# Optimization experiments

Measured on AMD Instinct MI355X. Metric: run time of the kernel, lower is better.

The kernel has to match this reference:

```python
import jax, jax.numpy as jnp
import numpy as np

jax.config.update("jax_enable_x64", True)  # torch lfilter runs in double precision

SR = 24000
RES_SIZE = 64
R_MIN, R_MAX = 0.9999, 0.99999
B, T = 4, 120000


def setup_inputs() -> dict:
    # Probe coefficients (fixed buffers, computed exactly as in Probe.__init__)
    theta_min = 2 * np.pi * 10.0 / SR
    theta_max = 2 * np.pi * 100.0 / SR
    theta = np.exp(np.linspace(np.log(theta_min), np.log(theta_max), RES_SIZE))
    radii = np.linspace(R_MIN, R_MAX, RES_SIZE)
    a1 = -2.0 * radii * np.cos(theta)          # [C]
    a2 = radii ** 2                             # [C]
    b0 = (1.0 - radii) * 0.5                    # [C]

    # Tank mixing weight: orthogonal init, shape [out=64, in=128] (rows orthonormal)
    rng = np.random.default_rng(1337)
    q, _ = np.linalg.qr(rng.standard_normal((2 * RES_SIZE, RES_SIZE)))  # [128,64], orthonormal cols
    W = q.T.astype(np.float32)                  # [64,128]

    key = jax.random.key(0)
    k1, k2 = jax.random.split(key)
    pred = jax.random.normal(k1, (B, 1, T), dtype=jnp.float32)
    target = jax.random.normal(k2, (B, 1, T), dtype=jnp.float32)
    return {
        "pred": pred,
        "target": target,
        "a1": jnp.asarray(a1, jnp.float64),
        "a2": jnp.asarray(a2, jnp.float64),
        "b0": jnp.asarray(b0, jnp.float64),
        "W": jnp.asarray(W, jnp.float32),
    }


def _biquad_bank(x, a1, a2, b0):
    """Biquad filter bank. x: [N, T] float64; coeffs: [C]. Returns [N, C, T].
    y[t] = b0*x[t] - a1*y[t-1] - a2*y[t-2]  (a0 = 1, b1 = b2 = 0, clamp=False)
    """
    n = x.shape[0]
    c = a1.shape[0]

    def step(carry, xt):
        y1, y2 = carry  # each [N, C]
        y = b0[None, :] * xt[:, None] - a1[None, :] * y1 - a2[None, :] * y2
        return (y, y1), y

    init = (jnp.zeros((n, c), x.dtype), jnp.zeros((n, c), x.dtype))
    _, ys = jax.lax.scan(step, init, x.T)      # [T, N, C]
    return jnp.transpose(ys, (1, 2, 0))        # [N, C, T]


def _probe(x, a1, a2, b0):
    """x: [B,1,T] float -> [B, 2C, T] float32 (fwd state ++ bwd state)."""
    xs = x[:, 0, :].astype(jnp.float64)        # [B, T]
    # run forward-time and reversed-time filters in one batched scan
    both = jnp.concatenate([xs, xs[:, ::-1]], axis=0)       # [2B, T]
    ys = _biquad_bank(both, a1, a2, b0)                      # [2B, C, T]
    nb = xs.shape[0]
    fwd_state = ys[:nb]                                      # [B, C, T]
    bwd_state = ys[nb:][:, :, ::-1]                          # [B, C, T] (flipped back)
    return jnp.concatenate([fwd_state, bwd_state], axis=1).astype(jnp.float32)


def _tank(x, W):
    """x: [B, 2C, T], W: [C, 2C] -> tanh(W @ x): [B, C, T]."""
    return jnp.tanh(jnp.einsum("bct,oc->bot", x, W))


def reference(pred, target, a1, a2, b0, W):
    t = pred.shape[-1]
    margin = t // 3
    p_emb = _tank(_probe(pred, a1, a2, b0), W)    # [B, C, T]
    t_emb = _tank(_probe(target, a1, a2, b0), W)  # [B, C, T]
    p_valid = p_emb[..., margin:t - margin]
    t_valid = t_emb[..., margin:t - margin]
    return jnp.mean(jnp.abs(p_valid - t_valid))
```

## Files before the change

kernel.cpp:

```cpp
#include <hip/hip_runtime.h>

#define T_LEN 120000
#define LBLK 160
#define PBLK 750
#define PB_USED 500
#define SEG_LEN 25
#define NSEG_USED 20
#define CCH 32
#define NCHUNK 5
#define BATCH 4
#define K0 250
#define NKV 250
#define DENOM 20480000.0
#define YSTR 130

typedef _Float16 half8 __attribute__((ext_vector_type(8)));
typedef float f32x4 __attribute__((ext_vector_type(4)));

__device__ __forceinline__ float fast_tanh(float x) {
  float e = __expf(2.0f * x);
  return 1.0f - 2.0f / (e + 1.0f);
}

__device__ __forceinline__ bool coeffs_are_f64(const void* a2p) {
  double probe = *(const double*)a2p;
  return probe > 0.9 && probe < 1.0;
}
__device__ __forceinline__ double coeff_d(const void* p, bool f64, int ch) {
  return f64 ? ((const double*)p)[ch] : (double)((const float*)p)[ch];
}

__device__ __forceinline__ void mat_pow(double A1, double A2, int e,
                                        double& r00, double& r01,
                                        double& r10, double& r11) {
  double m00 = -A1, m01 = -A2, m10 = 1.0, m11 = 0.0;
  r00 = 1.0; r01 = 0.0; r10 = 0.0; r11 = 1.0;
  while (e) {
    if (e & 1) {
      double t00 = r00 * m00 + r01 * m10, t01 = r00 * m01 + r01 * m11;
      double t10 = r10 * m00 + r11 * m10, t11 = r10 * m01 + r11 * m11;
      r00 = t00; r01 = t01; r10 = t10; r11 = t11;
    }
    e >>= 1;
    if (e) {
      double t00 = m00 * m00 + m01 * m10, t01 = m00 * m01 + m01 * m11;
      double t10 = m10 * m00 + m11 * m10, t11 = m10 * m01 + m11 * m11;
      m00 = t00; m01 = t01; m10 = t10; m11 = t11;
    }
  }
}

__global__ __launch_bounds__(64) void pass1(
    const float* __restrict__ pred, const float* __restrict__ tgt,
    const void* a1p, const void* a2p, const void* b0p,
    double* __restrict__ fbuf, double* __restrict__ wsum)
{
  if ((blockIdx.x | blockIdx.y) == 0 && threadIdx.x == 0) {
    wsum[0] = 0.0;
    ((unsigned int*)(wsum + 1))[0] = 0u;
  }
  int k = blockIdx.x, r = blockIdx.y;
  int i = r >> 3, d = (r >> 2) & 1, b = r & 3;
  const float* sig = (i ? tgt : pred) + b * T_LEN;
  __shared__ float xs[LBLK];
  int base = k * LBLK;
  for (int j = threadIdx.x; j < LBLK; j += 64)
    xs[j] = d ? sig[T_LEN - 1 - (base + j)] : sig[base + j];
  __syncthreads();
  int ch = threadIdx.x;
  bool f64 = coeffs_are_f64(a2p);
  float A1 = (float)coeff_d(a1p, f64, ch);
  float A2 = (float)coeff_d(a2p, f64, ch);
  float B0 = (float)coeff_d(b0p, f64, ch);
  float y1 = 0.0f, y2 = 0.0f;
  for (int j = 0; j < LBLK; ++j) {
    float y = fmaf(-A1, y1, fmaf(-A2, y2, B0 * xs[j]));
    y2 = y1; y1 = y;
  }
  int s = r * 64 + ch;
  ((double2*)fbuf)[(size_t)k * 1024 + s] = make_double2((double)y1, (double)y2);
}

__global__ __launch_bounds__(64) void pass2a(
    const void* a1p, const void* a2p,
    const double* __restrict__ fbuf, double* __restrict__ sbuf)
{
  int seg = blockIdx.x >> 4;
  int s = ((blockIdx.x & 15) << 6) + threadIdx.x;
  int ch = s & 63;
  bool f64 = coeffs_are_f64(a2p);
  double r00, r01, r10, r11;
  mat_pow(coeff_d(a1p, f64, ch), coeff_d(a2p, f64, ch), LBLK, r00, r01, r10, r11);
  const double2* fb = (const double2*)fbuf;
  double y1 = 0.0, y2 = 0.0;
  for (int jj = 0; jj < SEG_LEN / 5; ++jj) {
    size_t kb = (size_t)(seg * SEG_LEN + jj * 5) * 1024 + s;
    double2 f0 = fb[kb], f1 = fb[kb + 1024], f2 = fb[kb + 2048],
            f3 = fb[kb + 3072], f4 = fb[kb + 4096];
    double n1, n2;
    n1 = r00*y1 + r01*y2 + f0.x; n2 = r10*y1 + r11*y2 + f0.y; y1=n1; y2=n2;
    n1 = r00*y1 + r01*y2 + f1.x; n2 = r10*y1 + r11*y2 + f1.y; y1=n1; y2=n2;
    n1 = r00*y1 + r01*y2 + f2.x; n2 = r10*y1 + r11*y2 + f2.y; y1=n1; y2=n2;
    n1 = r00*y1 + r01*y2 + f3.x; n2 = r10*y1 + r11*y2 + f3.y; y1=n1; y2=n2;
    n1 = r00*y1 + r01*y2 + f4.x; n2 = r10*y1 + r11*y2 + f4.y; y1=n1; y2=n2;
  }
  ((double2*)sbuf)[(size_t)seg * 1024 + s] = make_double2(y1, y2);
}

__global__ __launch_bounds__(256, 4) void pass3(
    const float* __restrict__ pred, const float* __restrict__ tgt,
    const void* a1p, const void* a2p, const void* b0p,
    const float* __restrict__ W, const double* __restrict__ fbuf,
    const double* __restrict__ sbuf, double* __restrict__ wsum,
    float* __restrict__ out)
{
  int k = K0 + blockIdx.x;
  int b = blockIdx.y;
  int tid = threadIdx.x;
  __shared__ __align__(16) _Float16 ys[2][64 * YSTR];
  __shared__ float red[4];

  int g = tid >> 6, lane = tid & 63;
  int gu = __builtin_amdgcn_readfirstlane(g);
  int iu = gu >> 1, du = gu & 1;
  int ch = lane;
  int n0 = gu * 16;
  int lm = lane & 15, quad = lane >> 4;

  bool f64 = coeffs_are_f64(a2p);
  double A1d = coeff_d(a1p, f64, ch), A2d = coeff_d(a2p, f64, ch);
  double B0d = coeff_d(b0p, f64, ch);
  float A1 = (float)A1d, A2 = (float)A2d, B0 = (float)B0d;
  float IA2 = (float)(1.0 / A2d);

  int m = du ? (PBLK - k) : k;
  int seg = m / SEG_LEN, j = m - seg * SEG_LEN;
  int s = (iu * 8 + du * 4 + b) * 64 + ch;

  double q00, q01, q10, q11;
  mat_pow(A1d, A2d, LBLK * SEG_LEN, q00, q01, q10, q11);
  double y1 = 0.0, y2 = 0.0;
  const double2* sb = (const double2*)sbuf;
  #pragma unroll 1
  for (int qq = 0; qq < NSEG_USED; qq += 5) {
    double2 f[5];
    #pragma unroll
    for (int p = 0; p < 5; ++p) f[p] = sb[(size_t)(qq + p) * 1024 + s];
    #pragma unroll
    for (int p = 0; p < 5; ++p) {
      if (qq + p < seg) {
        double n1 = q00 * y1 + q01 * y2 + f[p].x;
        double n2 = q10 * y1 + q11 * y2 + f[p].y;
        y1 = n1; y2 = n2;
      }
    }
  }

  double r00, r01, r10, r11;
  mat_pow(A1d, A2d, LBLK, r00, r01, r10, r11);
  const double2* fb = (const double2*)fbuf;
  #pragma unroll 1
  for (int bb = 0; bb < 24; bb += 8) {
    double2 f[8];
    #pragma unroll
    for (int q = 0; q < 8; ++q) {
      int blk = seg * SEG_LEN + bb + q;
      if (blk >= PB_USED) blk = PB_USED - 1;
      f[q] = fb[(size_t)blk * 1024 + s];
    }
    #pragma unroll
    for (int q = 0; q < 8; ++q) {
      if (bb + q < j) {
        double n1 = r00 * y1 + r01 * y2 + f[q].x;
        double n2 = r10 * y1 + r11 * y2 + f[q].y;
        y1 = n1; y2 = n2;
      }
    }
  }
  float st0 = (float)y1, st1 = (float)y2;

  half8 wf[4][4];
  #pragma unroll
  for (int m0 = 0; m0 < 4; ++m0) {
    #pragma unroll
    for (int k0 = 0; k0 < 4; ++k0) {
      const float* wp = W + (m0 * 16 + lm) * 128 + k0 * 32 + quad * 8;
      float4 wa = *(const float4*)wp, wb = *(const float4*)(wp + 4);
      half8 h;
      h[0] = (_Float16)wa.x; h[1] = (_Float16)wa.y;
      h[2] = (_Float16)wa.z; h[3] = (_Float16)wa.w;
      h[4] = (_Float16)wb.x; h[5] = (_Float16)wb.y;
      h[6] = (_Float16)wb.z; h[7] = (_Float16)wb.w;
      wf[m0][k0] = h;
    }
  }

  const float* xp = (iu ? tgt : pred) + b * T_LEN + k * LBLK;

  float loss = 0.0f;
  for (int cc = 0; cc < NCHUNK; ++cc) {
    _Float16* yb = ys[cc & 1];
    if (du == 0) {
      #pragma unroll
      for (int tt = 0; tt < CCH; ++tt) {
        float x = xp[cc * CCH + tt];
        float y = fmaf(-A1, st0, fmaf(-A2, st1, B0 * x));
        yb[(2 * tt + iu) * YSTR + ch] = (_Float16)y;
        st1 = st0; st0 = y;
      }
    } else {
      #pragma unroll
      for (int tt = 0; tt < CCH; ++tt) {
        float x = xp[cc * CCH + tt];
        yb[(2 * tt + iu) * YSTR + 64 + ch] = (_Float16)st0;
        float ym2 = (fmaf(-A1, st1, B0 * x) - st0) * IA2;
        st0 = st1; st1 = ym2;
      }
    }
    __syncthreads();

    const _Float16* yrow = &yb[(n0 + lm) * YSTR + quad * 8];
    half8 bf0 = *(const half8*)(yrow);
    half8 bf1 = *(const half8*)(yrow + 32);
    half8 bf2 = *(const half8*)(yrow + 64);
    half8 bf3 = *(const half8*)(yrow + 96);
    #pragma unroll
    for (int m0 = 0; m0 < 4; ++m0) {
      f32x4 c = {0.f, 0.f, 0.f, 0.f};
      c = __builtin_amdgcn_mfma_f32_16x16x32_f16(wf[m0][0], bf0, c, 0, 0, 0);
      c = __builtin_amdgcn_mfma_f32_16x16x32_f16(wf[m0][1], bf1, c, 0, 0, 0);
      c = __builtin_amdgcn_mfma_f32_16x16x32_f16(wf[m0][2], bf2, c, 0, 0, 0);
      c = __builtin_amdgcn_mfma_f32_16x16x32_f16(wf[m0][3], bf3, c, 0, 0, 0);
      #pragma unroll
      for (int r = 0; r < 4; ++r) {
        float vv = fast_tanh(c[r]);
        float p = __shfl_xor(vv, 1);
        loss += fabsf(vv - p);
      }
    }
  }

  #pragma unroll
  for (int off = 32; off > 0; off >>= 1) loss += __shfl_down(loss, off);
  if (lane == 0) red[g] = loss;
  __syncthreads();
  if (tid == 0) {
    float blk = (red[0] + red[1]) + (red[2] + red[3]);
    atomicAdd(wsum, (double)blk);
    __threadfence();
    unsigned int n = atomicAdd((unsigned int*)(wsum + 1), 1u);
    if (n == (unsigned int)(NKV * BATCH - 1)) {
      __threadfence();
      double tot = atomicAdd(wsum, 0.0);
      out[0] = (float)(tot / DENOM);
    }
  }
}

extern "C" void kernel_launch(void* const* d_in, const int* in_sizes, int n_in,
                              void* d_out, int out_size, void* d_ws, size_t ws_size,
                              hipStream_t stream) {
  const float* pred = (const float*)d_in[0];
  const float* tgt  = (const float*)d_in[1];
  const void* a1p = d_in[2];
  const void* a2p = d_in[3];
  const void* b0p = d_in[4];
  const float* W  = (const float*)d_in[5];
  float* out = (float*)d_out;

  double* base = (double*)d_ws;
  double* wsum = base;
  double* fbuf = base + 8;
  double* sbuf = fbuf + (size_t)PB_USED * 1024 * 2;

  pass1<<<dim3(PB_USED, 16), 64, 0, stream>>>(pred, tgt, a1p, a2p, b0p,
                                              fbuf, wsum);
  pass2a<<<NSEG_USED * 16, 64, 0, stream>>>(a1p, a2p, fbuf, sbuf);
  pass3<<<dim3(NKV, BATCH), 256, 0, stream>>>(pred, tgt, a1p, a2p, b0p,
                                              W, fbuf, sbuf, wsum, out);
}
```

Baseline: 126.9 us.

## Precompute transition matrix powers once in pass2a and widen pass1 blocks

Block 0 of pass2a now computes the per-channel 160-step and 4000-step transition matrices and stores them in a small workspace table. Pass3 loads these instead of running two double-precision matrix-power loops in every block. Pass1 now packs four row groups into each 256-thread block rather than using 64-thread blocks, which cuts the block count by four. The risk is a little extra serial work in one pass2a block, plus a new dependency on a workspace region placed after sbuf.

```diff
diff --git a/kernel.cpp b/kernel.cpp
--- a/kernel.cpp
+++ b/kernel.cpp
@@ -50,7 +50,7 @@
   }
 }
 
-__global__ __launch_bounds__(64) void pass1(
+__global__ __launch_bounds__(256) void pass1(
     const float* __restrict__ pred, const float* __restrict__ tgt,
     const void* a1p, const void* a2p, const void* b0p,
     double* __restrict__ fbuf, double* __restrict__ wsum)
@@ -59,22 +59,25 @@
     wsum[0] = 0.0;
     ((unsigned int*)(wsum + 1))[0] = 0u;
   }
-  int k = blockIdx.x, r = blockIdx.y;
+  int k = blockIdx.x;
+  int g = threadIdx.x >> 6, lane = threadIdx.x & 63;
+  int gu = __builtin_amdgcn_readfirstlane(g);
+  int r = blockIdx.y * 4 + gu;
   int i = r >> 3, d = (r >> 2) & 1, b = r & 3;
   const float* sig = (i ? tgt : pred) + b * T_LEN;
-  __shared__ float xs[LBLK];
+  __shared__ float xs[4][LBLK];
   int base = k * LBLK;
-  for (int j = threadIdx.x; j < LBLK; j += 64)
-    xs[j] = d ? sig[T_LEN - 1 - (base + j)] : sig[base + j];
+  for (int j = lane; j < LBLK; j += 64)
+    xs[gu][j] = d ? sig[T_LEN - 1 - (base + j)] : sig[base + j];
   __syncthreads();
-  int ch = threadIdx.x;
+  int ch = lane;
   bool f64 = coeffs_are_f64(a2p);
   float A1 = (float)coeff_d(a1p, f64, ch);
   float A2 = (float)coeff_d(a2p, f64, ch);
   float B0 = (float)coeff_d(b0p, f64, ch);
   float y1 = 0.0f, y2 = 0.0f;
   for (int j = 0; j < LBLK; ++j) {
-    float y = fmaf(-A1, y1, fmaf(-A2, y2, B0 * xs[j]));
+    float y = fmaf(-A1, y1, fmaf(-A2, y2, B0 * xs[gu][j]));
     y2 = y1; y1 = y;
   }
   int s = r * 64 + ch;
@@ -83,7 +86,8 @@
 
 __global__ __launch_bounds__(64) void pass2a(
     const void* a1p, const void* a2p,
-    const double* __restrict__ fbuf, double* __restrict__ sbuf)
+    const double* __restrict__ fbuf, double* __restrict__ sbuf,
+    double* __restrict__ atab)
 {
   int seg = blockIdx.x >> 4;
   int s = ((blockIdx.x & 15) << 6) + threadIdx.x;
@@ -105,14 +109,36 @@
     n1 = r00*y1 + r01*y2 + f4.x; n2 = r10*y1 + r11*y2 + f4.y; y1=n1; y2=n2;
   }
   ((double2*)sbuf)[(size_t)seg * 1024 + s] = make_double2(y1, y2);
+
+  if (blockIdx.x == 0) {
+    double p00 = 1.0, p01 = 0.0, p10 = 0.0, p11 = 1.0;
+    double b00 = r00, b01 = r01, b10 = r10, b11 = r11;
+    int e = SEG_LEN;
+    while (e) {
+      if (e & 1) {
+        double t00 = p00*b00 + p01*b10, t01 = p00*b01 + p01*b11;
+        double t10 = p10*b00 + p11*b10, t11 = p10*b01 + p11*b11;
+        p00 = t00; p01 = t01; p10 = t10; p11 = t11;
+      }
+      e >>= 1;
+      if (e) {
+        double t00 = b00*b00 + b01*b10, t01 = b00*b01 + b01*b11;
+        double t10 = b10*b00 + b11*b10, t11 = b10*b01 + b11*b11;
+        b00 = t00; b01 = t01; b10 = t10; b11 = t11;
+      }
+    }
+    double* ap = atab + ch * 8;
+    ap[0] = r00; ap[1] = r01; ap[2] = r10; ap[3] = r11;
+    ap[4] = p00; ap[5] = p01; ap[6] = p10; ap[7] = p11;
+  }
 }
 
 __global__ __launch_bounds__(256, 4) void pass3(
     const float* __restrict__ pred, const float* __restrict__ tgt,
     const void* a1p, const void* a2p, const void* b0p,
     const float* __restrict__ W, const double* __restrict__ fbuf,
-    const double* __restrict__ sbuf, double* __restrict__ wsum,
-    float* __restrict__ out)
+    const double* __restrict__ sbuf, const double* __restrict__ atab,
+    double* __restrict__ wsum, float* __restrict__ out)
 {
   int k = K0 + blockIdx.x;
   int b = blockIdx.y;
@@ -133,12 +159,15 @@
   float A1 = (float)A1d, A2 = (float)A2d, B0 = (float)B0d;
   float IA2 = (float)(1.0 / A2d);
 
+  const double2* ap = (const double2*)(atab + ch * 8);
+  double2 ra = ap[0], rb = ap[1], qa = ap[2], qb = ap[3];
+  double r00 = ra.x, r01 = ra.y, r10 = rb.x, r11 = rb.y;
+  double q00 = qa.x, q01 = qa.y, q10 = qb.x, q11 = qb.y;
+
   int m = du ? (PBLK - k) : k;
   int seg = m / SEG_LEN, j = m - seg * SEG_LEN;
   int s = (iu * 8 + du * 4 + b) * 64 + ch;
 
-  double q00, q01, q10, q11;
-  mat_pow(A1d, A2d, LBLK * SEG_LEN, q00, q01, q10, q11);
   double y1 = 0.0, y2 = 0.0;
   const double2* sb = (const double2*)sbuf;
   #pragma unroll 1
@@ -156,8 +185,6 @@
     }
   }
 
-  double r00, r01, r10, r11;
-  mat_pow(A1d, A2d, LBLK, r00, r01, r10, r11);
   const double2* fb = (const double2*)fbuf;
   #pragma unroll 1
   for (int bb = 0; bb < 24; bb += 8) {
@@ -272,10 +299,11 @@
   double* wsum = base;
   double* fbuf = base + 8;
   double* sbuf = fbuf + (size_t)PB_USED * 1024 * 2;
-
-  pass1<<<dim3(PB_USED, 16), 64, 0, stream>>>(pred, tgt, a1p, a2p, b0p,
+  double* atab = sbuf + (size_t)32 * 1024 * 2;
+
+  pass1<<<dim3(PB_USED, 4), 256, 0, stream>>>(pred, tgt, a1p, a2p, b0p,
                                               fbuf, wsum);
-  pass2a<<<NSEG_USED * 16, 64, 0, stream>>>(a1p, a2p, fbuf, sbuf);
+  pass2a<<<NSEG_USED * 16, 64, 0, stream>>>(a1p, a2p, fbuf, sbuf, atab);
   pass3<<<dim3(NKV, BATCH), 256, 0, stream>>>(pred, tgt, a1p, a2p, b0p,
-                                              W, fbuf, sbuf, wsum, out);
-}
+                                              W, fbuf, sbuf, atab, wsum, out);
+}
```

Measured after the change: 126.9 us. About the same (+0.0%).
